# Kernel optimization log

Measured on AMD Instinct MI355X. Metric: run time of the kernel, lower is better.

## Reference

```python
import jax, jax.numpy as jnp
import numpy as np

DIM = 128
POS_HID = 64
ATT_HID = DIM * 2
B, N = 4, 512


def _linear_init(key, fan_in, fan_out):
    # mimic torch Linear default init scale: U(-1/sqrt(fan_in), 1/sqrt(fan_in))
    kw, kb = jax.random.split(key)
    bound = 1.0 / np.sqrt(fan_in)
    W = jax.random.uniform(kw, (fan_in, fan_out), minval=-bound, maxval=bound, dtype=jnp.float32)
    b = jax.random.uniform(kb, (fan_out,), minval=-bound, maxval=bound, dtype=jnp.float32)
    return W, b


def setup_inputs() -> dict:
    key = jax.random.key(0)
    ks = jax.random.split(key, 6)
    x = jax.random.normal(ks[0], (B, DIM, N), dtype=jnp.float32)
    pos = jax.random.normal(ks[1], (B, N, 3), dtype=jnp.float32)
    Wqkv, bqkv = _linear_init(ks[2], DIM, DIM * 3)
    pW1, pb1 = _linear_init(ks[3], 3, POS_HID)
    pW2, pb2 = _linear_init(ks[4], POS_HID, DIM)
    k5a, k5b = jax.random.split(ks[5])
    aW1, ab1 = _linear_init(k5a, DIM, ATT_HID)
    aW2, ab2 = _linear_init(k5b, ATT_HID, DIM)
    return {"x": x, "pos": pos, "Wqkv": Wqkv, "bqkv": bqkv,
            "pW1": pW1, "pb1": pb1, "pW2": pW2, "pb2": pb2,
            "aW1": aW1, "ab1": ab1, "aW2": aW2, "ab2": ab2}


def reference(x, pos, Wqkv, bqkv, pW1, pb1, pW2, pb2, aW1, ab1, aW2, ab2):
    # x: [b, d, n] -> [b, n, d]
    xt = jnp.transpose(x, (0, 2, 1))
    qkv = xt @ Wqkv + bqkv                      # [b, n, 3d]
    q, k, v = jnp.split(qkv, 3, axis=-1)        # each [b, n, d]

    # pairwise relative positions: [b, i, j, 3]
    rel_pos = pos[:, :, None, :] - pos[:, None, :, :]
    # pos_mlp: Linear(3, hid) -> ReLU -> Linear(hid, d)
    rel_pos_emb = jax.nn.relu(rel_pos @ pW1 + pb1) @ pW2 + pb2   # [b, i, j, d]

    qk_rel = q[:, :, None, :] - k[:, None, :, :]                 # [b, i, j, d]
    v_ij = v[:, None, :, :] + rel_pos_emb                        # [b, i, j, d]

    # attn_mlp: Linear(d, 2d) -> ReLU -> Linear(2d, d)
    sim = jax.nn.relu((qk_rel + rel_pos_emb) @ aW1 + ab1) @ aW2 + ab2  # [b, i, j, d]
    attn = jax.nn.softmax(sim, axis=2)                           # softmax over j (dim=-2)
    agg = jnp.sum(attn * v_ij, axis=2)                           # [b, i, d]
    return jnp.transpose(agg, (0, 2, 1))                         # [b, d, n]
```

## Files before the change

kernel.cpp:

```cpp
#include <hip/hip_runtime.h>
#include <hip/hip_bf16.h>

#define B_ 4
#define N_ 512
#define D_ 128
#define LOG2E 1.4426950408889634f

typedef __attribute__((ext_vector_type(8))) short bf16x8;
typedef __attribute__((ext_vector_type(4))) short s16x4;
typedef __attribute__((ext_vector_type(4))) float f32x4;
typedef __attribute__((ext_vector_type(16))) float f32x16;

__device__ __forceinline__ f32x4 mfma16(bf16x8 a, bf16x8 b, f32x4 c) {
    return __builtin_amdgcn_mfma_f32_16x16x32_bf16(a, b, c, 0, 0, 0);
}
__device__ __forceinline__ f32x16 mfma32(bf16x8 a, bf16x8 b, f32x16 c) {
    return __builtin_amdgcn_mfma_f32_32x32x16_bf16(a, b, c, 0, 0, 0);
}
__device__ __forceinline__ short bf16b(float x) {
    __hip_bfloat16 h = __float2bfloat16(x);
    return *reinterpret_cast<short*>(&h);
}
__device__ __forceinline__ float b2f(short s) {
    unsigned u = ((unsigned)(unsigned short)s) << 16;
    union { unsigned u; float f; } c; c.u = u; return c.f;
}

__global__ void prep_weights_kernel(const float* __restrict__ aW1, const float* __restrict__ aW2,
                                    const float* __restrict__ pW2, const float* __restrict__ pb2,
                                    const float* __restrict__ ab1,
                                    __hip_bfloat16* __restrict__ aW2T, __hip_bfloat16* __restrict__ pW2T,
                                    __hip_bfloat16* __restrict__ W12T, float* __restrict__ cvec) {
    int idx = blockIdx.x * 256 + threadIdx.x;
    if (idx < 128 * 256) {
        int n = idx >> 8, k2 = idx & 255;
        aW2T[idx] = __float2bfloat16(aW2[k2 * 128 + n] * LOG2E);
    }
    if (idx < 128 * 64) {
        int n = idx >> 6, k2 = idx & 63;
        pW2T[idx] = __float2bfloat16(pW2[k2 * 128 + n]);
    }
    if (idx < 256 * 64) {
        int n = idx >> 6, h = idx & 63;
        float s = 0.f;
#pragma unroll 8
        for (int d = 0; d < 128; ++d) s += pW2[h * 128 + d] * aW1[d * 256 + n];
        W12T[idx] = __float2bfloat16(s);
    }
    if (idx < 256) {
        float s = ab1[idx];
#pragma unroll 8
        for (int d = 0; d < 128; ++d) s += pb2[d] * aW1[d * 256 + idx];
        cvec[idx] = s;
    }
}

__global__ void posw_kernel(const float* __restrict__ pos, const float* __restrict__ pW1,
                            float* __restrict__ posw) {
    int idx = blockIdx.x * 256 + threadIdx.x;
    int t = idx >> 6, h = idx & 63;
    float p0 = pos[t * 3 + 0], p1 = pos[t * 3 + 1], p2 = pos[t * 3 + 2];
    posw[idx] = p0 * pW1[h] + p1 * pW1[64 + h] + p2 * pW1[128 + h];
}

__global__ void qkv_kernel(const float* __restrict__ x, const float* __restrict__ Wqkv,
                           const float* __restrict__ bqkv,
                           float* __restrict__ q, float* __restrict__ k,
                           short* __restrict__ vb_t) {
    int idx = blockIdx.x * 256 + threadIdx.x;
    int m = idx % 384;
    int g = idx / 384;
    int bn0 = g * 4;
    int b = bn0 >> 9, n0 = bn0 & (N_ - 1);
    const float* xp = x + (b * D_) * N_ + n0;
    float bias = bqkv[m];
    float a0 = bias, a1 = bias, a2 = bias, a3 = bias;
#pragma unroll 4
    for (int d = 0; d < D_; ++d) {
        float wv = Wqkv[d * 384 + m];
        const float4 xv = *reinterpret_cast<const float4*>(xp + d * N_);
        a0 = fmaf(xv.x, wv, a0); a1 = fmaf(xv.y, wv, a1);
        a2 = fmaf(xv.z, wv, a2); a3 = fmaf(xv.w, wv, a3);
    }
    if (m < 256) {
        int mm = m & 127;
        float* dst = (m < 128) ? q : k;
        dst[(bn0 + 0) * D_ + mm] = a0;
        dst[(bn0 + 1) * D_ + mm] = a1;
        dst[(bn0 + 2) * D_ + mm] = a2;
        dst[(bn0 + 3) * D_ + mm] = a3;
    } else {
        int d = m & 127;
        int jt = n0 >> 6;
        int jr = n0 & 63;
        int rt = jr >> 5;
        int jrr = jr & 31;
        int rb = 4 * (jrr >> 3);
        int hi = (jrr >> 2) & 1;
        int lane = (d & 31) + 32 * hi;
        int ct = d >> 5;
        s16x4 pk;
        pk[0] = bf16b(a0); pk[1] = bf16b(a1); pk[2] = bf16b(a2); pk[3] = bf16b(a3);
        size_t base = (size_t)b * 65536 + (size_t)jt * 8192 + ((rt * 4 + ct) * 64 + lane) * 16 + rb;
        *(s16x4*)(vb_t + base) = pk;
    }
}

__global__ void qka_kernel(const float* __restrict__ q, const float* __restrict__ k,
                           const float* __restrict__ aW1,
                           float* __restrict__ qa, short* __restrict__ kab_t) {
    int col = threadIdx.x;
    int bn0 = blockIdx.x * 4;
    int b = bn0 >> 9, n0 = bn0 & (N_ - 1);
    const float* qp = q + bn0 * D_;
    const float* kp = k + bn0 * D_;
    float aq0 = 0, aq1 = 0, aq2 = 0, aq3 = 0;
    float ak0 = 0, ak1 = 0, ak2 = 0, ak3 = 0;
#pragma unroll 4
    for (int d = 0; d < D_; ++d) {
        float wv = aW1[d * 256 + col];
        aq0 = fmaf(qp[d], wv, aq0);        ak0 = fmaf(kp[d], wv, ak0);
        aq1 = fmaf(qp[D_ + d], wv, aq1);   ak1 = fmaf(kp[D_ + d], wv, ak1);
        aq2 = fmaf(qp[2*D_ + d], wv, aq2); ak2 = fmaf(kp[2*D_ + d], wv, ak2);
        aq3 = fmaf(qp[3*D_ + d], wv, aq3); ak3 = fmaf(kp[3*D_ + d], wv, ak3);
    }
    qa[(bn0 + 0) * 256 + col] = aq0;
    qa[(bn0 + 1) * 256 + col] = aq1;
    qa[(bn0 + 2) * 256 + col] = aq2;
    qa[(bn0 + 3) * 256 + col] = aq3;
    int jt = n0 >> 6;
    int mt = (n0 >> 4) & 3;
    int lg = (n0 >> 2) & 3;
    int w  = col >> 5, nt = (col >> 4) & 1, lc = col & 15;
    int l  = lg * 16 + lc;
    s16x4 pk;
    pk[0] = bf16b(ak0); pk[1] = bf16b(ak1); pk[2] = bf16b(ak2); pk[3] = bf16b(ak3);
    size_t base = (((((size_t)b * 8 + jt) * 8 + w) * 2 + nt) * 4 + mt) * 256 + l * 4;
    *(s16x4*)(kab_t + base) = pk;
}

__global__ __launch_bounds__(512, 2) void fused_attn_kernel(
    const float* __restrict__ qa, const short* __restrict__ kab_t,
    const short* __restrict__ vb_t,
    const float* __restrict__ posw, const float* __restrict__ pb1,
    const __hip_bfloat16* __restrict__ pW2T, const float* __restrict__ pb2,
    const __hip_bfloat16* __restrict__ W12T, const float* __restrict__ cvec,
    const __hip_bfloat16* __restrict__ aW2T, const float* __restrict__ ab2,
    float* __restrict__ out)
{
    __shared__ __hip_bfloat16 ph_s[64][72];
    __shared__ __hip_bfloat16 hid_s[64][264];
    __shared__ float pwi_s[64];
    __shared__ float mrg_s[4][32][4];

    const int tid = threadIdx.x;
    const int w   = tid >> 6;
    const int l   = tid & 63;
    const int lg  = l >> 4;
    const int lc  = l & 15;
    const int l31 = l & 31;
    const int hi  = l >> 5;
    const int rt  = w >> 2;
    const int ct  = w & 3;
    const int gx8 = ((l31 >> 2) & 3) << 3;

    const int bi = (blockIdx.x & 7) * 256 + (blockIdx.x >> 3);
    const int b  = bi >> 9;
    const int i  = bi & (N_ - 1);

    if (tid < 64) pwi_s[tid] = posw[(size_t)(b * N_ + i) * 64 + tid] + pb1[tid];

    const int col0  = 32 * w + lc;
    const int dcol2 = 32 * ct + l31;

    const float qrow0 = qa[(b * N_ + i) * 256 + col0] + cvec[col0];
    const float qrow1 = qa[(b * N_ + i) * 256 + col0 + 16] + cvec[col0 + 16];
    const float ab2_r = ab2[dcol2] * LOG2E;
    const float pb2_r = pb2[dcol2];

    const __hip_bfloat16* a2base = aW2T + (size_t)dcol2 * 256 + 8 * hi;
    bf16x8 bw2[16];
#pragma unroll
    for (int ks = 0; ks < 16; ++ks)
        bw2[ks] = *(const bf16x8*)(a2base + 16 * ks);
    bf16x8 bwp[4];
    {
        const __hip_bfloat16* ppb = pW2T + (size_t)dcol2 * 64 + 8 * hi;
#pragma unroll
        for (int ks = 0; ks < 4; ++ks)
            bwp[ks] = *(const bf16x8*)(ppb + 16 * ks);
    }
    bf16x8 bw12[2][2];
#pragma unroll
    for (int nt = 0; nt < 2; ++nt)
#pragma unroll
        for (int k2 = 0; k2 < 2; ++k2)
            bw12[nt][k2] = *(const bf16x8*)(W12T + (size_t)(32 * w + 16 * nt + lc) * 64 + k2 * 32 + 8 * lg);

    float m_run = -1e30f, l_run = 0.f, o_run = 0.f;

    const short* ktp0 = kab_t + (size_t)b * 131072 + w * 2048 + l * 4;
    const short* vtp0 = vb_t + (size_t)b * 65536 + ((rt * 4 + ct) * 64 + l) * 16;

    __syncthreads();

    for (int jt = 0; jt < 8; ++jt) {
        const int jb = jt * 64;

        {
            const int jl = tid >> 3;
            const int hb = (tid & 7) * 8;
            const float* pj = posw + (size_t)(b * N_ + jb + jl) * 64 + hb;
            float4 x0 = *(const float4*)pj;
            float4 x1 = *(const float4*)(pj + 4);
            bf16x8 tv;
            tv[0] = bf16b(fmaxf(pwi_s[hb + 0] - x0.x, 0.f));
            tv[1] = bf16b(fmaxf(pwi_s[hb + 1] - x0.y, 0.f));
            tv[2] = bf16b(fmaxf(pwi_s[hb + 2] - x0.z, 0.f));
            tv[3] = bf16b(fmaxf(pwi_s[hb + 3] - x0.w, 0.f));
            tv[4] = bf16b(fmaxf(pwi_s[hb + 4] - x1.x, 0.f));
            tv[5] = bf16b(fmaxf(pwi_s[hb + 5] - x1.y, 0.f));
            tv[6] = bf16b(fmaxf(pwi_s[hb + 6] - x1.z, 0.f));
            tv[7] = bf16b(fmaxf(pwi_s[hb + 7] - x1.w, 0.f));
            *(bf16x8*)(&ph_s[jl][hb]) = tv;
        }
        __syncthreads();

        const short* vtp = vtp0 + (size_t)jt * 8192;
        const short* ktp = ktp0 + (size_t)jt * 16384;
        s16x4 vb4[4];
#pragma unroll
        for (int q4 = 0; q4 < 4; ++q4)
            vb4[q4] = *(const s16x4*)(vtp + 4 * q4);
        s16x4 kv[2][4];
#pragma unroll
        for (int nt = 0; nt < 2; ++nt)
#pragma unroll
            for (int mt = 0; mt < 4; ++mt)
                kv[nt][mt] = *(const s16x4*)(ktp + nt * 1024 + mt * 256);

        float vv[16];
        {
            f32x16 accr = {0.f,0.f,0.f,0.f,0.f,0.f,0.f,0.f,0.f,0.f,0.f,0.f,0.f,0.f,0.f,0.f};
#pragma unroll
            for (int ks = 0; ks < 4; ++ks) {
                bf16x8 a = *(const bf16x8*)(&ph_s[32 * rt + l31][16 * ks + 8 * hi]);
                accr = mfma32(a, bwp[ks], accr);
            }
#pragma unroll
            for (int r = 0; r < 16; ++r)
                vv[r] = accr[r] + b2f(vb4[r >> 2][r & 3]) + pb2_r;
        }

        {
#pragma unroll
            for (int mt = 0; mt < 4; ++mt) {
                bf16x8 a0 = *(const bf16x8*)(&ph_s[mt * 16 + lc][8 * lg]);
                bf16x8 a1 = *(const bf16x8*)(&ph_s[mt * 16 + lc][32 + 8 * lg]);
#pragma unroll
                for (int nt = 0; nt < 2; ++nt) {
                    f32x4 acc = {0.f, 0.f, 0.f, 0.f};
                    acc = mfma16(a0, bw12[nt][0], acc);
                    acc = mfma16(a1, bw12[nt][1], acc);
                    const float qv = nt ? qrow1 : qrow0;
                    const int colw = 32 * w + (((16 * nt + lc) ^ (8 * lg)) & 31);
#pragma unroll
                    for (int r = 0; r < 4; ++r) {
                        int row = mt * 16 + 4 * lg + r;
                        hid_s[row][colw] = __float2bfloat16(
                            fmaxf(acc[r] + qv - b2f(kv[nt][mt][r]), 0.f));
                    }
                }
            }
        }
        __syncthreads();

        f32x16 acc2a = {0.f,0.f,0.f,0.f,0.f,0.f,0.f,0.f,0.f,0.f,0.f,0.f,0.f,0.f,0.f,0.f};
        f32x16 acc2b = {0.f,0.f,0.f,0.f,0.f,0.f,0.f,0.f,0.f,0.f,0.f,0.f,0.f,0.f,0.f,0.f};
        {
            const short* hrow = (const short*)&hid_s[32 * rt + l31][0];
#pragma unroll
            for (int ks = 0; ks < 8; ++ks) {
                bf16x8 aa = *(const bf16x8*)(hrow + ((16 * ks + 8 * hi) ^ gx8));
                bf16x8 ab = *(const bf16x8*)(hrow + ((16 * (ks + 8) + 8 * hi) ^ gx8));
                acc2a = mfma32(aa, bw2[ks], acc2a);
                acc2b = mfma32(ab, bw2[ks + 8], acc2b);
            }
        }

        {
#pragma unroll
            for (int r = 0; r < 16; ++r) acc2a[r] += acc2b[r];
            float t8[8];
#pragma unroll
            for (int r = 0; r < 8; ++r) t8[r] = fmaxf(acc2a[r], acc2a[r + 8]);
            float t4a = fmaxf(t8[0], t8[4]), t4b = fmaxf(t8[1], t8[5]);
            float t4c = fmaxf(t8[2], t8[6]), t4d = fmaxf(t8[3], t8[7]);
            float tmax = fmaxf(fmaxf(t4a, t4b), fmaxf(t4c, t4d));
            float m_new = fmaxf(m_run, tmax + ab2_r);
            float mm = m_new - ab2_r;
            float scale = __builtin_amdgcn_exp2f(m_run - m_new);
            l_run *= scale;
            o_run *= scale;
#pragma unroll
            for (int r = 0; r < 16; ++r) {
                float e = __builtin_amdgcn_exp2f(acc2a[r] - mm);
                l_run += e;
                o_run = fmaf(e, vv[r], o_run);
            }
            m_run = m_new;
        }
    }

    float m2 = __shfl_xor(m_run, 32);
    float l2 = __shfl_xor(l_run, 32);
    float o2 = __shfl_xor(o_run, 32);
    float M1 = fmaxf(m_run, m2);
    float e1 = __builtin_amdgcn_exp2f(m_run - M1);
    float e2 = __builtin_amdgcn_exp2f(m2 - M1);
    float L1 = l_run * e1 + l2 * e2;
    float O1 = o_run * e1 + o2 * e2;

    if (rt == 1 && hi == 0) {
        mrg_s[ct][l31][0] = M1;
        mrg_s[ct][l31][1] = L1;
        mrg_s[ct][l31][2] = O1;
    }
    __syncthreads();
    if (rt == 0 && hi == 0) {
        float Mb = mrg_s[ct][l31][0];
        float Lb = mrg_s[ct][l31][1];
        float Ob = mrg_s[ct][l31][2];
        float M = fmaxf(M1, Mb);
        float ea = __builtin_amdgcn_exp2f(M1 - M);
        float eb = __builtin_amdgcn_exp2f(Mb - M);
        float L = L1 * ea + Lb * eb;
        float O = O1 * ea + Ob * eb;
        out[((size_t)b * D_ + dcol2) * N_ + i] = O / L;
    }
}

extern "C" void kernel_launch(void* const* d_in, const int* in_sizes, int n_in,
                              void* d_out, int out_size, void* d_ws, size_t ws_size,
                              hipStream_t stream) {
    const float* x    = (const float*)d_in[0];
    const float* pos  = (const float*)d_in[1];
    const float* Wqkv = (const float*)d_in[2];
    const float* bqkv = (const float*)d_in[3];
    const float* pW1  = (const float*)d_in[4];
    const float* pb1  = (const float*)d_in[5];
    const float* pW2  = (const float*)d_in[6];
    const float* pb2  = (const float*)d_in[7];
    const float* aW1  = (const float*)d_in[8];
    const float* ab1  = (const float*)d_in[9];
    const float* aW2  = (const float*)d_in[10];
    const float* ab2  = (const float*)d_in[11];
    float* out = (float*)d_out;

    float* q    = (float*)d_ws;
    float* k    = q  + B_ * N_ * D_;
    float* qa   = k  + B_ * N_ * D_;
    float* posw = qa + B_ * N_ * 256;
    float* cvec = posw + B_ * N_ * 64;
    short* kab_t = (short*)(cvec + 256);
    short* vb_t  = kab_t + B_ * N_ * 256;
    __hip_bfloat16* aW2T = (__hip_bfloat16*)(vb_t + B_ * N_ * D_);
    __hip_bfloat16* pW2T = aW2T + 128 * 256;
    __hip_bfloat16* W12T = pW2T + 128 * 64;

    hipLaunchKernelGGL(prep_weights_kernel, dim3(128), dim3(256), 0, stream,
                       aW1, aW2, pW2, pb2, ab1, aW2T, pW2T, W12T, cvec);
    hipLaunchKernelGGL(posw_kernel, dim3(512), dim3(256), 0, stream,
                       pos, pW1, posw);
    hipLaunchKernelGGL(qkv_kernel, dim3(768), dim3(256), 0, stream,
                       x, Wqkv, bqkv, q, k, vb_t);
    hipLaunchKernelGGL(qka_kernel, dim3(512), dim3(256), 0, stream,
                       q, k, aW1, qa, kab_t);
    hipLaunchKernelGGL(fused_attn_kernel, dim3(2048), dim3(512), 0, stream,
                       qa, kab_t, vb_t, posw, pb1, pW2T, pb2, W12T, cvec, aW2T, ab2, out);
}
```

Baseline: 259.7 us.

## Process two query rows per block to reuse loaded K/V and weight registers

Each block now handles two consecutive query rows i instead of one, halving the grid to 1024 blocks. The per-j-tile loads of posw, kab_t and vb_t, and the register-resident weight fragments, are shared across both rows, which cuts global memory traffic and per-block setup. In exchange, LDS use roughly doubles (ph_s and hid_s are duplicated) and register pressure rises (vv[2][16] plus duplicated softmax state), which may hurt occupancy under the 512x2 launch bounds. The grid is also halved, so there are fewer blocks per CU.

```diff
diff --git a/kernel.cpp b/kernel.cpp
--- a/kernel.cpp
+++ b/kernel.cpp
@@ -148,10 +148,10 @@
     const __hip_bfloat16* __restrict__ aW2T, const float* __restrict__ ab2,
     float* __restrict__ out)
 {
-    __shared__ __hip_bfloat16 ph_s[64][72];
-    __shared__ __hip_bfloat16 hid_s[64][264];
-    __shared__ float pwi_s[64];
-    __shared__ float mrg_s[4][32][4];
+    __shared__ __hip_bfloat16 ph_s[2][64][72];
+    __shared__ __hip_bfloat16 hid_s[2][64][264];
+    __shared__ float pwi_s[2][64];
+    __shared__ float mrg_s[2][4][32][4];
 
     const int tid = threadIdx.x;
     const int w   = tid >> 6;
@@ -164,17 +164,22 @@
     const int ct  = w & 3;
     const int gx8 = ((l31 >> 2) & 3) << 3;
 
-    const int bi = (blockIdx.x & 7) * 256 + (blockIdx.x >> 3);
-    const int b  = bi >> 9;
-    const int i  = bi & (N_ - 1);
-
-    if (tid < 64) pwi_s[tid] = posw[(size_t)(b * N_ + i) * 64 + tid] + pb1[tid];
+    const int blk = (blockIdx.x & 7) * 128 + (blockIdx.x >> 3);
+    const int b   = blk >> 8;
+    const int i0  = (blk & 255) * 2;
+
+    if (tid < 128) {
+        int ii = tid >> 6, h = tid & 63;
+        pwi_s[ii][h] = posw[(size_t)(b * N_ + i0 + ii) * 64 + h] + pb1[h];
+    }
 
     const int col0  = 32 * w + lc;
     const int dcol2 = 32 * ct + l31;
 
-    const float qrow0 = qa[(b * N_ + i) * 256 + col0] + cvec[col0];
-    const float qrow1 = qa[(b * N_ + i) * 256 + col0 + 16] + cvec[col0 + 16];
+    const float qr00 = qa[(b * N_ + i0) * 256 + col0] + cvec[col0];
+    const float qr01 = qa[(b * N_ + i0) * 256 + col0 + 16] + cvec[col0 + 16];
+    const float qr10 = qa[(b * N_ + i0 + 1) * 256 + col0] + cvec[col0];
+    const float qr11 = qa[(b * N_ + i0 + 1) * 256 + col0 + 16] + cvec[col0 + 16];
     const float ab2_r = ab2[dcol2] * LOG2E;
     const float pb2_r = pb2[dcol2];
 
@@ -197,7 +202,10 @@
         for (int k2 = 0; k2 < 2; ++k2)
             bw12[nt][k2] = *(const bf16x8*)(W12T + (size_t)(32 * w + 16 * nt + lc) * 64 + k2 * 32 + 8 * lg);
 
-    float m_run = -1e30f, l_run = 0.f, o_run = 0.f;
+    float m_run[2] = {-1e30f, -1e30f};
+    float l_run[2] = {0.f, 0.f};
+    float o_run[2] = {0.f, 0.f};
+    float vv[2][16];
 
     const short* ktp0 = kab_t + (size_t)b * 131072 + w * 2048 + l * 4;
     const short* vtp0 = vb_t + (size_t)b * 65536 + ((rt * 4 + ct) * 64 + l) * 16;
@@ -213,16 +221,15 @@
             const float* pj = posw + (size_t)(b * N_ + jb + jl) * 64 + hb;
             float4 x0 = *(const float4*)pj;
             float4 x1 = *(const float4*)(pj + 4);
-            bf16x8 tv;
-            tv[0] = bf16b(fmaxf(pwi_s[hb + 0] - x0.x, 0.f));
-            tv[1] = bf16b(fmaxf(pwi_s[hb + 1] - x0.y, 0.f));
-            tv[2] = bf16b(fmaxf(pwi_s[hb + 2] - x0.z, 0.f));
-            tv[3] = bf16b(fmaxf(pwi_s[hb + 3] - x0.w, 0.f));
-            tv[4] = bf16b(fmaxf(pwi_s[hb + 4] - x1.x, 0.f));
-            tv[5] = bf16b(fmaxf(pwi_s[hb + 5] - x1.y, 0.f));
-            tv[6] = bf16b(fmaxf(pwi_s[hb + 6] - x1.z, 0.f));
-            tv[7] = bf16b(fmaxf(pwi_s[hb + 7] - x1.w, 0.f));
-            *(bf16x8*)(&ph_s[jl][hb]) = tv;
+            float xr[8] = {x0.x, x0.y, x0.z, x0.w, x1.x, x1.y, x1.z, x1.w};
+#pragma unroll
+            for (int ii = 0; ii < 2; ++ii) {
+                bf16x8 tv;
+#pragma unroll
+                for (int h = 0; h < 8; ++h)
+                    tv[h] = bf16b(fmaxf(pwi_s[ii][hb + h] - xr[h], 0.f));
+                *(bf16x8*)(&ph_s[ii][jl][hb]) = tv;
+            }
         }
         __syncthreads();
 
@@ -239,35 +246,36 @@
             for (int mt = 0; mt < 4; ++mt)
                 kv[nt][mt] = *(const s16x4*)(ktp + nt * 1024 + mt * 256);
 
-        float vv[16];
-        {
+#pragma unroll
+        for (int ii = 0; ii < 2; ++ii) {
             f32x16 accr = {0.f,0.f,0.f,0.f,0.f,0.f,0.f,0.f,0.f,0.f,0.f,0.f,0.f,0.f,0.f,0.f};
 #pragma unroll
             for (int ks = 0; ks < 4; ++ks) {
-                bf16x8 a = *(const bf16x8*)(&ph_s[32 * rt + l31][16 * ks + 8 * hi]);
+                bf16x8 a = *(const bf16x8*)(&ph_s[ii][32 * rt + l31][16 * ks + 8 * hi]);
                 accr = mfma32(a, bwp[ks], accr);
             }
 #pragma unroll
             for (int r = 0; r < 16; ++r)
-                vv[r] = accr[r] + b2f(vb4[r >> 2][r & 3]) + pb2_r;
-        }
-
-        {
+                vv[ii][r] = accr[r] + b2f(vb4[r >> 2][r & 3]) + pb2_r;
+        }
+
+#pragma unroll
+        for (int ii = 0; ii < 2; ++ii) {
 #pragma unroll
             for (int mt = 0; mt < 4; ++mt) {
-                bf16x8 a0 = *(const bf16x8*)(&ph_s[mt * 16 + lc][8 * lg]);
-                bf16x8 a1 = *(const bf16x8*)(&ph_s[mt * 16 + lc][32 + 8 * lg]);
+                bf16x8 a0 = *(const bf16x8*)(&ph_s[ii][mt * 16 + lc][8 * lg]);
+                bf16x8 a1 = *(const bf16x8*)(&ph_s[ii][mt * 16 + lc][32 + 8 * lg]);
 #pragma unroll
                 for (int nt = 0; nt < 2; ++nt) {
                     f32x4 acc = {0.f, 0.f, 0.f, 0.f};
                     acc = mfma16(a0, bw12[nt][0], acc);
                     acc = mfma16(a1, bw12[nt][1], acc);
-                    const float qv = nt ? qrow1 : qrow0;
+                    const float qv = ii ? (nt ? qr11 : qr10) : (nt ? qr01 : qr00);
                     const int colw = 32 * w + (((16 * nt + lc) ^ (8 * lg)) & 31);
 #pragma unroll
                     for (int r = 0; r < 4; ++r) {
                         int row = mt * 16 + 4 * lg + r;
-                        hid_s[row][colw] = __float2bfloat16(
+                        hid_s[ii][row][colw] = __float2bfloat16(
                             fmaxf(acc[r] + qv - b2f(kv[nt][mt][r]), 0.f));
                     }
                 }
@@ -275,10 +283,11 @@
         }
         __syncthreads();
 
-        f32x16 acc2a = {0.f,0.f,0.f,0.f,0.f,0.f,0.f,0.f,0.f,0.f,0.f,0.f,0.f,0.f,0.f,0.f};
-        f32x16 acc2b = {0.f,0.f,0.f,0.f,0.f,0.f,0.f,0.f,0.f,0.f,0.f,0.f,0.f,0.f,0.f,0.f};
-        {
-            const short* hrow = (const short*)&hid_s[32 * rt + l31][0];
+#pragma unroll
+        for (int ii = 0; ii < 2; ++ii) {
+            f32x16 acc2a = {0.f,0.f,0.f,0.f,0.f,0.f,0.f,0.f,0.f,0.f,0.f,0.f,0.f,0.f,0.f,0.f};
+            f32x16 acc2b = {0.f,0.f,0.f,0.f,0.f,0.f,0.f,0.f,0.f,0.f,0.f,0.f,0.f,0.f,0.f,0.f};
+            const short* hrow = (const short*)&hid_s[ii][32 * rt + l31][0];
 #pragma unroll
             for (int ks = 0; ks < 8; ++ks) {
                 bf16x8 aa = *(const bf16x8*)(hrow + ((16 * ks + 8 * hi) ^ gx8));
@@ -286,9 +295,6 @@
                 acc2a = mfma32(aa, bw2[ks], acc2a);
                 acc2b = mfma32(ab, bw2[ks + 8], acc2b);
             }
-        }
-
-        {
 #pragma unroll
             for (int r = 0; r < 16; ++r) acc2a[r] += acc2b[r];
             float t8[8];
@@ -297,46 +303,52 @@
             float t4a = fmaxf(t8[0], t8[4]), t4b = fmaxf(t8[1], t8[5]);
             float t4c = fmaxf(t8[2], t8[6]), t4d = fmaxf(t8[3], t8[7]);
             float tmax = fmaxf(fmaxf(t4a, t4b), fmaxf(t4c, t4d));
-            float m_new = fmaxf(m_run, tmax + ab2_r);
+            float m_new = fmaxf(m_run[ii], tmax + ab2_r);
             float mm = m_new - ab2_r;
-            float scale = __builtin_amdgcn_exp2f(m_run - m_new);
-            l_run *= scale;
-            o_run *= scale;
+            float scale = __builtin_amdgcn_exp2f(m_run[ii] - m_new);
+            l_run[ii] *= scale;
+            o_run[ii] *= scale;
 #pragma unroll
             for (int r = 0; r < 16; ++r) {
                 float e = __builtin_amdgcn_exp2f(acc2a[r] - mm);
-                l_run += e;
-                o_run = fmaf(e, vv[r], o_run);
-            }
-            m_run = m_new;
-        }
-    }
-
-    float m2 = __shfl_xor(m_run, 32);
-    float l2 = __shfl_xor(l_run, 32);
-    float o2 = __shfl_xor(o_run, 32);
-    float M1 = fmaxf(m_run, m2);
-    float e1 = __builtin_amdgcn_exp2f(m_run - M1);
-    float e2 = __builtin_amdgcn_exp2f(m2 - M1);
-    float L1 = l_run * e1 + l2 * e2;
-    float O1 = o_run * e1 + o2 * e2;
-
-    if (rt == 1 && hi == 0) {
-        mrg_s[ct][l31][0] = M1;
-        mrg_s[ct][l31][1] = L1;
-        mrg_s[ct][l31][2] = O1;
+                l_run[ii] += e;
+                o_run[ii] = fmaf(e, vv[ii][r], o_run[ii]);
+            }
+            m_run[ii] = m_new;
+        }
+    }
+
+    float M1[2], L1[2], O1[2];
+#pragma unroll
+    for (int ii = 0; ii < 2; ++ii) {
+        float m2 = __shfl_xor(m_run[ii], 32);
+        float l2 = __shfl_xor(l_run[ii], 32);
+        float o2 = __shfl_xor(o_run[ii], 32);
+        M1[ii] = fmaxf(m_run[ii], m2);
+        float e1 = __builtin_amdgcn_exp2f(m_run[ii] - M1[ii]);
+        float e2 = __builtin_amdgcn_exp2f(m2 - M1[ii]);
+        L1[ii] = l_run[ii] * e1 + l2 * e2;
+        O1[ii] = o_run[ii] * e1 + o2 * e2;
+        if (rt == 1 && hi == 0) {
+            mrg_s[ii][ct][l31][0] = M1[ii];
+            mrg_s[ii][ct][l31][1] = L1[ii];
+            mrg_s[ii][ct][l31][2] = O1[ii];
+        }
     }
     __syncthreads();
     if (rt == 0 && hi == 0) {
-        float Mb = mrg_s[ct][l31][0];
-        float Lb = mrg_s[ct][l31][1];
-        float Ob = mrg_s[ct][l31][2];
-        float M = fmaxf(M1, Mb);
-        float ea = __builtin_amdgcn_exp2f(M1 - M);
-        float eb = __builtin_amdgcn_exp2f(Mb - M);
-        float L = L1 * ea + Lb * eb;
-        float O = O1 * ea + Ob * eb;
-        out[((size_t)b * D_ + dcol2) * N_ + i] = O / L;
+#pragma unroll
+        for (int ii = 0; ii < 2; ++ii) {
+            float Mb = mrg_s[ii][ct][l31][0];
+            float Lb = mrg_s[ii][ct][l31][1];
+            float Ob = mrg_s[ii][ct][l31][2];
+            float M = fmaxf(M1[ii], Mb);
+            float ea = __builtin_amdgcn_exp2f(M1[ii] - M);
+            float eb = __builtin_amdgcn_exp2f(Mb - M);
+            float L = L1[ii] * ea + Lb * eb;
+            float O = O1[ii] * ea + Ob * eb;
+            out[((size_t)b * D_ + dcol2) * N_ + i0 + ii] = O / L;
+        }
     }
 }
 
@@ -376,6 +388,6 @@
                        x, Wqkv, bqkv, q, k, vb_t);
     hipLaunchKernelGGL(qka_kernel, dim3(512), dim3(256), 0, stream,
                        q, k, aW1, qa, kab_t);
-    hipLaunchKernelGGL(fused_attn_kernel, dim3(2048), dim3(512), 0, stream,
+    hipLaunchKernelGGL(fused_attn_kernel, dim3(1024), dim3(512), 0, stream,
                        qa, kab_t, vb_t, posw, pb1, pW2T, pb2, W12T, cvec, aW2T, ab2, out);
 }
```

Measured after the change: 219.9 us. -15.3%, faster.
